# Kernel tuning notes

Hardware: AMD Instinct MI355X
Metric: run time of the kernel (lower is better)

Reference implementation:

```python
import jax, jax.numpy as jnp
from jax import lax
import numpy as np

NPOINT, RADIUS, NSAMPLE = 1024, 0.2, 32
MLP = [64, 64, 128]
IN_CH = 35  # 3 coord channels + 32 point features
EPS = 1e-5


def farthest_point_sample(xyz, npoint):
    # xyz: (B, N, 3) -> (B, npoint) int32. Deterministic start at index 0.
    B, N, _ = xyz.shape

    def step(carry, _):
        dist, farthest = carry  # (B,N), (B,)
        centroid = jnp.take_along_axis(xyz, farthest[:, None, None], axis=1)  # (B,1,3)
        d = jnp.sum((xyz - centroid) ** 2, axis=-1)  # (B,N)
        dist = jnp.minimum(dist, d)
        nxt = jnp.argmax(dist, axis=-1).astype(jnp.int32)
        return (dist, nxt), farthest

    init = (jnp.full((B, N), 1e10, xyz.dtype), jnp.zeros((B,), jnp.int32))
    _, idxs = lax.scan(step, init, None, length=npoint)
    return idxs.T  # (B, npoint)


def gather_points(points, idx):
    # points: (B, N, C); idx: (B, ...) int -> (B, ..., C)
    return jax.vmap(lambda p, i: p[i])(points, idx)


def query_ball_point(radius, nsample, xyz, new_xyz):
    # xyz: (B,N,3), new_xyz: (B,S,3) -> (B,S,nsample) int32
    B, N, _ = xyz.shape
    sqrdists = jnp.sum((new_xyz[:, :, None, :] - xyz[:, None, :, :]) ** 2, axis=-1)  # (B,S,N)
    group_idx = jnp.where(sqrdists > radius ** 2, N, jnp.arange(N, dtype=jnp.int32))
    group_idx = jnp.sort(group_idx, axis=-1)[:, :, :nsample]
    first = group_idx[:, :, :1]
    return jnp.where(group_idx == N, first, group_idx)


def sa_forward(xyz, points, params):
    B, N, C = xyz.shape
    fps_idx = farthest_point_sample(xyz, NPOINT)
    new_xyz = gather_points(xyz, fps_idx)  # (B,S,3)
    idx = query_ball_point(RADIUS, NSAMPLE, xyz, new_xyz)  # (B,S,K)
    grouped_xyz = gather_points(xyz, idx)  # (B,S,K,3)
    grouped_xyz_norm = grouped_xyz - new_xyz[:, :, None, :]
    grouped_points = gather_points(points, idx)  # (B,S,K,D)
    new_points = jnp.concatenate([grouped_xyz_norm, grouped_points], axis=-1)  # (B,S,K,Cin)
    x = new_points.transpose(0, 3, 2, 1)  # (B, Cin, K, S)
    for w, b, g, be in params:
        x = jnp.einsum('oi,biks->boks', w, x) + b[None, :, None, None]  # 1x1 conv
        mean = x.mean(axis=(0, 2, 3), keepdims=True)  # BatchNorm2d, training mode
        var = x.var(axis=(0, 2, 3), keepdims=True)
        x = (x - mean) / jnp.sqrt(var + EPS)
        x = jax.nn.relu(g[None, :, None, None] * x + be[None, :, None, None])
    new_points_out = x.max(axis=2)  # max over nsample -> (B, Cout, S)
    return new_xyz, new_points_out


def setup_inputs() -> dict:
    key = jax.random.key(0)
    ks = jax.random.split(key, 16)
    B, N, D = 16, 4096, 32
    inp = {
        'xyz': jax.random.uniform(ks[0], (B, N, 3), dtype=jnp.float32),
        'points': jax.random.normal(ks[1], (B, N, D), dtype=jnp.float32),
    }
    last = IN_CH
    for li, out_ch in enumerate(MLP):
        inp[f'w{li}'] = jax.random.normal(ks[2 + 4 * li], (out_ch, last), dtype=jnp.float32) * 0.05
        inp[f'b{li}'] = jnp.zeros((out_ch,), jnp.float32)
        inp[f'g{li}'] = jnp.ones((out_ch,), jnp.float32)
        inp[f'be{li}'] = jnp.zeros((out_ch,), jnp.float32)
        last = out_ch
    return inp


def reference(xyz, points, w0, b0, g0, be0, w1, b1, g1, be1, w2, b2, g2, be2):
    params = [(w0, b0, g0, be0), (w1, b1, g1, be1), (w2, b2, g2, be2)]
    return sa_forward(xyz, points, params)
```

## Files before the change

kernel.cpp:

```cpp
#include <hip/hip_runtime.h>
#include <hip/hip_bf16.h>
#include <stdint.h>

#pragma clang fp contract(off)

#define BATCH   16
#define NPTS    4096
#define NPOINT  1024
#define NSAMPLE 32
#define NPOS    (BATCH*NPOINT*NSAMPLE)
#define NBLK    (NPOS/128)
#define NGRP    (BATCH*NPOINT)
#define EPSV    1e-5f

typedef unsigned short ushort_t;
typedef unsigned int uint_t;
typedef unsigned long long u64;
typedef __attribute__((ext_vector_type(8))) short bf16x8;
typedef __attribute__((ext_vector_type(4))) float f32x4;
typedef __attribute__((ext_vector_type(2))) float f32x2;

__device__ inline ushort_t f2bf(float f) {
    uint_t u = __float_as_uint(f);
    u += 0x7fffu + ((u >> 16) & 1u);
    return (ushort_t)(u >> 16);
}
__device__ inline uint_t pkbf(float a, float b) {
    __hip_bfloat162 h = __float22bfloat162_rn(make_float2(a, b));
    uint_t r; __builtin_memcpy(&r, &h, 4); return r;
}
__device__ inline bf16x8 asbf(uint4 u) {
    bf16x8 v; __builtin_memcpy(&v, &u, 16); return v;
}
__device__ inline void unpack8(uint4 u, float* f) {
    f[0] = __uint_as_float(u.x << 16); f[1] = __uint_as_float(u.x & 0xffff0000u);
    f[2] = __uint_as_float(u.y << 16); f[3] = __uint_as_float(u.y & 0xffff0000u);
    f[4] = __uint_as_float(u.z << 16); f[5] = __uint_as_float(u.z & 0xffff0000u);
    f[6] = __uint_as_float(u.w << 16); f[7] = __uint_as_float(u.w & 0xffff0000u);
}

__global__ __launch_bounds__(256) void prep_w(const float* __restrict__ w0,
                                              const float* __restrict__ w1,
                                              const float* __restrict__ w2,
                                              ushort_t* __restrict__ Wp0,
                                              ushort_t* __restrict__ Wx0,
                                              ushort_t* __restrict__ Wp1,
                                              ushort_t* __restrict__ Wp2) {
    const int t = blockIdx.x * 256 + threadIdx.x;
    const int stride = gridDim.x * 256;
    for (int i = t; i < 64 * 32; i += stride) { int ch = i >> 5, k = i & 31; Wp0[i] = f2bf(w0[ch * 35 + 3 + k]); }
    for (int i = t; i < 64 * 4;  i += stride) { int ch = i >> 2, q = i & 3;  Wx0[i] = (q < 3) ? f2bf(w0[ch * 35 + q]) : (ushort_t)0; }
    for (int i = t; i < 64 * 64; i += stride) Wp1[i] = f2bf(w1[i]);
    for (int i = t; i < 128 * 64; i += stride) Wp2[i] = f2bf(w2[i]);
}

#define DPP_MAX_STAGE(CTRL) do {                                              \
    uint_t _lo2 = __builtin_amdgcn_update_dpp(lo, lo, CTRL, 0xf, 0xf, false); \
    uint_t _hi2 = __builtin_amdgcn_update_dpp(hi, hi, CTRL, 0xf, 0xf, false); \
    u64 _o = ((u64)_hi2 << 32) | _lo2;                                        \
    u64 _v = ((u64)hi << 32) | lo;                                            \
    bool _g = _o > _v;                                                        \
    lo = _g ? _lo2 : lo; hi = _g ? _hi2 : hi;                                 \
} while (0)

__global__ __launch_bounds__(256) void fps_kernel(const float* __restrict__ xyz,
                                                  float* __restrict__ new_xyz) {
    __shared__ float4 lxyz[NPTS];
    __shared__ u64 wbest[2][4];
    __shared__ int fpsidx[NPOINT];
    const int b = blockIdx.x;
    const int tid = threadIdx.x;
    const float* base = xyz + (size_t)b * NPTS * 3;
    for (int n = tid; n < NPTS; n += 256) {
        lxyz[n] = make_float4(base[3 * n], base[3 * n + 1], base[3 * n + 2], 0.f);
    }
    __syncthreads();

    f32x2 px[8], py[8], pz[8], dist[8];
    uint_t lowc[16];
#pragma unroll
    for (int j = 0; j < 8; j++) {
// ... 51 lines not shown
        u64 b2 = wbest[par][2], b3 = wbest[par][3];
        u64 m01 = b0 > b1 ? b0 : b1;
        u64 m23 = b2 > b3 ? b2 : b3;
        u64 bb = m01 > m23 ? m01 : m23;
        cur = (int)(~(uint_t)bb) & (NPTS - 1);
        if (tid == 0) fpsidx[it] = cur;
    }
    __syncthreads();
    float* ob = new_xyz + (size_t)b * NPOINT * 3;
    for (int s = tid; s < NPOINT; s += 256) {
        float4 v = lxyz[fpsidx[s]];
        ob[3 * s + 0] = v.x; ob[3 * s + 1] = v.y; ob[3 * s + 2] = v.z;
    }
}

__global__ __launch_bounds__(256) void ballq_kernel(const float* __restrict__ xyz,
                                                    const float* __restrict__ new_xyz,
                                                    int* __restrict__ gidx) {
    const int gw = (int)((blockIdx.x * 256 + threadIdx.x) >> 6);
    const int lane = threadIdx.x & 63;
    const int b = gw / NPOINT, s = gw % NPOINT;
    const float* nb = new_xyz + ((size_t)b * NPOINT + s) * 3;
    const float cx = nb[0], cy = nb[1], cz = nb[2];
    const float* xb = xyz + (size_t)b * NPTS * 3;
    const float r2 = (float)(0.2 * 0.2);
    int cnt = 0;
    int first = -1;
    int* out = gidx + (size_t)gw * NSAMPLE;
    for (int j0 = 0; j0 < NPTS; j0 += 64) {
        int j = j0 + lane;
        float dx = __fsub_rn(xb[j * 3 + 0], cx);
        float dy = __fsub_rn(xb[j * 3 + 1], cy);
        float dz = __fsub_rn(xb[j * 3 + 2], cz);
        float d = __fadd_rn(__fadd_rn(__fmul_rn(dx, dx), __fmul_rn(dy, dy)),
                            __fmul_rn(dz, dz));
        bool pred = !(d > r2);
        u64 mask = __ballot(pred);
        if (first < 0 && mask != 0ull) first = j0 + (__ffsll((long long)mask) - 1);
        int before = __popcll(mask & ((1ull << lane) - 1ull));
        int slot = cnt + before;
        if (pred && slot < NSAMPLE) out[slot] = j;
        cnt += (int)__popcll(mask);
        if (cnt >= NSAMPLE) break;
    }
    if (cnt < NSAMPLE) {
        if (lane >= cnt && lane < NSAMPLE) out[lane] = first;
    }
}

__global__ __launch_bounds__(256) void conv1_mfma(const float* __restrict__ xyz,
                                                  const float* __restrict__ points,
                                                  const float* __restrict__ new_xyz,
                                                  const int* __restrict__ gidx,
                                                  const ushort_t* __restrict__ Wp0,
                                                  const ushort_t* __restrict__ Wx0,
                                                  const float* __restrict__ bias,
                                                  ushort_t* __restrict__ Y,
                                                  float* __restrict__ part_s,
                                                  float* __restrict__ part_q) {
    const int lane = threadIdx.x & 63, wid = threadIdx.x >> 6;
    const int l15 = lane & 15, quad = lane >> 4;
    const int p0 = blockIdx.x * 128 + wid * 32;

    bf16x8 Bp[4], Bx[4];
#pragma unroll
    for (int nt = 0; nt < 4; nt++) {
        const int ch = nt * 16 + l15;
        Bp[nt] = *(const bf16x8*)(Wp0 + (size_t)ch * 32 + quad * 8);
        uint4 bx = {0u, 0u, 0u, 0u};
        if (quad == 0) {
            uint2 wv = *(const uint2*)(Wx0 + ch * 4);
            bx.x = wv.x; bx.y = wv.y;
        }
        Bx[nt] = asbf(bx);
    }
    f32x4 acc[2][4];
#pragma unroll
    for (int mt = 0; mt < 2; mt++)
#pragma unroll
        for (int nt = 0; nt < 4; nt++) acc[mt][nt] = (f32x4){0.f, 0.f, 0.f, 0.f};

#pragma unroll
    for (int mt = 0; mt < 2; mt++) {
        const int p = p0 + mt * 16 + l15;
        const int b = p >> 15, s = (p & 32767) >> 5;
        const int j = gidx[p];
        const float* pr = points + ((size_t)(b * NPTS + j)) * 32 + quad * 8;
        float4 pa = *(const float4*)pr;
        float4 pb4 = *(const float4*)(pr + 4);
        uint4 ap;
        ap.x = pkbf(pa.x, pa.y);  ap.y = pkbf(pa.z, pa.w);
        ap.z = pkbf(pb4.x, pb4.y); ap.w = pkbf(pb4.z, pb4.w);
        bf16x8 Ap = asbf(ap);
        uint4 ax = {0u, 0u, 0u, 0u};
        if (quad == 0) {
            const float* xp = xyz + ((size_t)(b * NPTS + j)) * 3;
            const float* nz = new_xyz + ((size_t)(b * NPOINT + s)) * 3;
            float d0 = xp[0] - nz[0], d1 = xp[1] - nz[1], d2 = xp[2] - nz[2];
            ax.x = pkbf(d0, d1);
            ax.y = pkbf(d2, 0.f);
        }
        bf16x8 Ax = asbf(ax);
#pragma unroll
        for (int nt = 0; nt < 4; nt++) {
            acc[mt][nt] = __builtin_amdgcn_mfma_f32_16x16x32_bf16(Ap, Bp[nt], acc[mt][nt], 0, 0, 0);
            acc[mt][nt] = __builtin_amdgcn_mfma_f32_16x16x32_bf16(Ax, Bx[nt], acc[mt][nt], 0, 0, 0);
        }
    }
    float s_[4], q_[4];
#pragma unroll
    for (int nt = 0; nt < 4; nt++) { s_[nt] = 0.f; q_[nt] = 0.f; }
#pragma unroll
    for (int nt = 0; nt < 4; nt++) {
        const int ch = nt * 16 + l15;
        const float bs = bias[ch];
#pragma unroll
        for (int mt = 0; mt < 2; mt++) {
            const int pb = p0 + mt * 16 + quad * 4;
            float x0 = acc[mt][nt][0] + bs, x1 = acc[mt][nt][1] + bs;
            float x2 = acc[mt][nt][2] + bs, x3 = acc[mt][nt][3] + bs;
            uint_t p01 = pkbf(x0, x1), p23 = pkbf(x2, x3);
            Y[(size_t)(pb + 0) * 64 + ch] = (ushort_t)(p01 & 0xffffu);
            Y[(size_t)(pb + 1) * 64 + ch] = (ushort_t)(p01 >> 16);
            Y[(size_t)(pb + 2) * 64 + ch] = (ushort_t)(p23 & 0xffffu);
            Y[(size_t)(pb + 3) * 64 + ch] = (ushort_t)(p23 >> 16);
            float v0 = __uint_as_float(p01 << 16), v1 = __uint_as_float(p01 & 0xffff0000u);
            float v2 = __uint_as_float(p23 << 16), v3 = __uint_as_float(p23 & 0xffff0000u);
            s_[nt] += (v0 + v1) + (v2 + v3);
            q_[nt] += (v0 * v0 + v1 * v1) + (v2 * v2 + v3 * v3);
        }
    }
#pragma unroll
    for (int nt = 0; nt < 4; nt++) {
        s_[nt] += __shfl_xor(s_[nt], 16, 64); s_[nt] += __shfl_xor(s_[nt], 32, 64);
        q_[nt] += __shfl_xor(q_[nt], 16, 64); q_[nt] += __shfl_xor(q_[nt], 32, 64);
    }
    __shared__ float reds[4][4][16], redq[4][4][16];
    if (lane < 16) {
#pragma unroll
        for (int nt = 0; nt < 4; nt++) { reds[wid][nt][lane] = s_[nt]; redq[wid][nt][lane] = q_[nt]; }
    }
    __syncthreads();
    if (threadIdx.x < 16) {
#pragma unroll
        for (int nt = 0; nt < 4; nt++) {
            float ss = 0.f, qq = 0.f;
#pragma unroll
            for (int w = 0; w < 4; w++) { ss += reds[w][nt][threadIdx.x]; qq += redq[w][nt][threadIdx.x]; }
            const int ch = nt * 16 + threadIdx.x;
            part_s[(size_t)ch * NBLK + blockIdx.x] = ss;
            part_q[(size_t)ch * NBLK + blockIdx.x] = qq;
        }
    }
}

__global__ __launch_bounds__(256) void conv2_mfma(const ushort_t* __restrict__ Yin,
                                                  const float* __restrict__ scale,
                                                  const float* __restrict__ shift,
                                                  const ushort_t* __restrict__ Wp,
                                                  const float* __restrict__ bias,
                                                  ushort_t* __restrict__ Yout,
                                                  float* __restrict__ part_s,
                                                  float* __restrict__ part_q) {
    constexpr int IN = 64, OUT = 64, NT = 4;
    const int lane = threadIdx.x & 63, wid = threadIdx.x >> 6;
    const int l15 = lane & 15, quad = lane >> 4;
    const int p0 = blockIdx.x * 128 + wid * 32;

    float sc[2][8], sh[2][8];
#pragma unroll
    for (int kq = 0; kq < 2; kq++) {
        const int i0 = kq * 32 + quad * 8;
#pragma unroll
        for (int q = 0; q < 8; q++) { sc[kq][q] = scale[i0 + q]; sh[kq][q] = shift[i0 + q]; }
    }
    bf16x8 Bf[NT][2];
#pragma unroll
    for (int nt = 0; nt < NT; nt++)
#pragma unroll
        for (int kq = 0; kq < 2; kq++)
            Bf[nt][kq] = *(const bf16x8*)(Wp + (size_t)(nt * 16 + l15) * IN + kq * 32 + quad * 8);

    bf16x8 Af[2][2];
#pragma unroll
    for (int mt = 0; mt < 2; mt++)
#pragma unroll
        for (int kq = 0; kq < 2; kq++) {
            const ushort_t* yr = Yin + (size_t)(p0 + mt * 16 + l15) * IN + kq * 32 + quad * 8;
            uint4 u = *(const uint4*)yr;
            float f[8]; unpack8(u, f);
            float g0 = fmaxf(fmaf(f[0], sc[kq][0], sh[kq][0]), 0.f);
            float g1 = fmaxf(fmaf(f[1], sc[kq][1], sh[kq][1]), 0.f);
            float g2 = fmaxf(fmaf(f[2], sc[kq][2], sh[kq][2]), 0.f);
            float g3 = fmaxf(fmaf(f[3], sc[kq][3], sh[kq][3]), 0.f);
            float g4 = fmaxf(fmaf(f[4], sc[kq][4], sh[kq][4]), 0.f);
            float g5 = fmaxf(fmaf(f[5], sc[kq][5], sh[kq][5]), 0.f);
            float g6 = fmaxf(fmaf(f[6], sc[kq][6], sh[kq][6]), 0.f);
            float g7 = fmaxf(fmaf(f[7], sc[kq][7], sh[kq][7]), 0.f);
            uint4 a;
            a.x = pkbf(g0, g1); a.y = pkbf(g2, g3);
            a.z = pkbf(g4, g5); a.w = pkbf(g6, g7);
            Af[mt][kq] = asbf(a);
        }

    f32x4 acc[2][NT];
#pragma unroll
    for (int mt = 0; mt < 2; mt++)
#pragma unroll
        for (int nt = 0; nt < NT; nt++) acc[mt][nt] = (f32x4){0.f, 0.f, 0.f, 0.f};
#pragma unroll
    for (int mt = 0; mt < 2; mt++)
#pragma unroll
        for (int nt = 0; nt < NT; nt++) {
            acc[mt][nt] = __builtin_amdgcn_mfma_f32_16x16x32_bf16(Af[mt][0], Bf[nt][0], acc[mt][nt], 0, 0, 0);
            acc[mt][nt] = __builtin_amdgcn_mfma_f32_16x16x32_bf16(Af[mt][1], Bf[nt][1], acc[mt][nt], 0, 0, 0);
        }
    float s_[NT], q_[NT];
#pragma unroll
    for (int nt = 0; nt < NT; nt++) { s_[nt] = 0.f; q_[nt] = 0.f; }
#pragma unroll
    for (int nt = 0; nt < NT; nt++) {
        const int ch = nt * 16 + l15;
        const float bs = bias[ch];
#pragma unroll
        for (int mt = 0; mt < 2; mt++) {
            const int pb = p0 + mt * 16 + quad * 4;
            float x0 = acc[mt][nt][0] + bs, x1 = acc[mt][nt][1] + bs;
            float x2 = acc[mt][nt][2] + bs, x3 = acc[mt][nt][3] + bs;
            uint_t p01 = pkbf(x0, x1), p23 = pkbf(x2, x3);
            Yout[(size_t)(pb + 0) * OUT + ch] = (ushort_t)(p01 & 0xffffu);
            Yout[(size_t)(pb + 1) * OUT + ch] = (ushort_t)(p01 >> 16);
            Yout[(size_t)(pb + 2) * OUT + ch] = (ushort_t)(p23 & 0xffffu);
            Yout[(size_t)(pb + 3) * OUT + ch] = (ushort_t)(p23 >> 16);
            float v0 = __uint_as_float(p01 << 16), v1 = __uint_as_float(p01 & 0xffff0000u);
            float v2 = __uint_as_float(p23 << 16), v3 = __uint_as_float(p23 & 0xffff0000u);
            s_[nt] += (v0 + v1) + (v2 + v3);
            q_[nt] += (v0 * v0 + v1 * v1) + (v2 * v2 + v3 * v3);
        }
    }
#pragma unroll
    for (int nt = 0; nt < NT; nt++) {
        s_[nt] += __shfl_xor(s_[nt], 16, 64); s_[nt] += __shfl_xor(s_[nt], 32, 64);
        q_[nt] += __shfl_xor(q_[nt], 16, 64); q_[nt] += __shfl_xor(q_[nt], 32, 64);
    }
    __shared__ float reds[4][NT][16], redq[4][NT][16];
    if (lane < 16) {
#pragma unroll
        for (int nt = 0; nt < NT; nt++) { reds[wid][nt][lane] = s_[nt]; redq[wid][nt][lane] = q_[nt]; }
    }
    __syncthreads();
    if (threadIdx.x < 16) {
#pragma unroll
        for (int nt = 0; nt < NT; nt++) {
            float ss = 0.f, qq = 0.f;
#pragma unroll
            for (int w = 0; w < 4; w++) { ss += reds[w][nt][threadIdx.x]; qq += redq[w][nt][threadIdx.x]; }
            const int ch = nt * 16 + threadIdx.x;
            part_s[(size_t)ch * NBLK + blockIdx.x] = ss;
            part_q[(size_t)ch * NBLK + blockIdx.x] = qq;
        }
    }
}

__global__ __launch_bounds__(256) void conv3_mfma(const ushort_t* __restrict__ Yin,
                                                  const float* __restrict__ scale,
                                                  const float* __restrict__ shift,
                                                  const ushort_t* __restrict__ Wp,
                                                  const float* __restrict__ bias,
                                                  float* __restrict__ xmax,
                                                  float* __restrict__ xmin,
                                                  float* __restrict__ part_s,
                                                  float* __restrict__ part_q) {
    constexpr int IN = 64, NT = 8;
    const int lane = threadIdx.x & 63, wid = threadIdx.x >> 6;
    const int l15 = lane & 15, quad = lane >> 4;
    const int p0 = blockIdx.x * 128 + wid * 32;
    const int g = p0 >> 5;

    float sc[2][8], sh[2][8];
#pragma unroll
    for (int kq = 0; kq < 2; kq++) {
        const int i0 = kq * 32 + quad * 8;
#pragma unroll
        for (int q = 0; q < 8; q++) { sc[kq][q] = scale[i0 + q]; sh[kq][q] = shift[i0 + q]; }
    }
    bf16x8 Bf[NT][2];
#pragma unroll
    for (int nt = 0; nt < NT; nt++)
#pragma unroll
        for (int kq = 0; kq < 2; kq++)
            Bf[nt][kq] = *(const bf16x8*)(Wp + (size_t)(nt * 16 + l15) * IN + kq * 32 + quad * 8);

    bf16x8 Af[2][2];
#pragma unroll
    for (int mt = 0; mt < 2; mt++)
#pragma unroll
        for (int kq = 0; kq < 2; kq++) {
            const ushort_t* yr = Yin + (size_t)(p0 + mt * 16 + l15) * IN + kq * 32 + quad * 8;
            uint4 u = *(const uint4*)yr;
            float f[8]; unpack8(u, f);
            float g0 = fmaxf(fmaf(f[0], sc[kq][0], sh[kq][0]), 0.f);
            float g1 = fmaxf(fmaf(f[1], sc[kq][1], sh[kq][1]), 0.f);
            float g2 = fmaxf(fmaf(f[2], sc[kq][2], sh[kq][2]), 0.f);
            float g3 = fmaxf(fmaf(f[3], sc[kq][3], sh[kq][3]), 0.f);
            float g4 = fmaxf(fmaf(f[4], sc[kq][4], sh[kq][4]), 0.f);
            float g5 = fmaxf(fmaf(f[5], sc[kq][5], sh[kq][5]), 0.f);
            float g6 = fmaxf(fmaf(f[6], sc[kq][6], sh[kq][6]), 0.f);
            float g7 = fmaxf(fmaf(f[7], sc[kq][7], sh[kq][7]), 0.f);
            uint4 a;
            a.x = pkbf(g0, g1); a.y = pkbf(g2, g3);
            a.z = pkbf(g4, g5); a.w = pkbf(g6, g7);
            Af[mt][kq] = asbf(a);
        }

    f32x4 acc[2][NT];
#pragma unroll
    for (int mt = 0; mt < 2; mt++)
#pragma unroll
        for (int nt = 0; nt < NT; nt++) acc[mt][nt] = (f32x4){0.f, 0.f, 0.f, 0.f};
#pragma unroll
    for (int mt = 0; mt < 2; mt++)
#pragma unroll
        for (int nt = 0; nt < NT; nt++) {
            acc[mt][nt] = __builtin_amdgcn_mfma_f32_16x16x32_bf16(Af[mt][0], Bf[nt][0], acc[mt][nt], 0, 0, 0);
            acc[mt][nt] = __builtin_amdgcn_mfma_f32_16x16x32_bf16(Af[mt][1], Bf[nt][1], acc[mt][nt], 0, 0, 0);
        }
    float s_[NT], q_[NT], xm[NT], xn[NT];
#pragma unroll
    for (int nt = 0; nt < NT; nt++) { s_[nt] = 0.f; q_[nt] = 0.f; xm[nt] = -3e38f; xn[nt] = 3e38f; }
#pragma unroll
    for (int nt = 0; nt < NT; nt++) {
        const float bs = bias[nt * 16 + l15];
#pragma unroll
        for (int mt = 0; mt < 2; mt++) {
#pragma unroll
            for (int r = 0; r < 4; r++) {
                float x = acc[mt][nt][r] + bs;
                s_[nt] += x; q_[nt] += x * x;
                xm[nt] = fmaxf(xm[nt], x); xn[nt] = fminf(xn[nt], x);
            }
        }
    }
#pragma unroll
    for (int nt = 0; nt < NT; nt++) {
        s_[nt] += __shfl_xor(s_[nt], 16, 64); s_[nt] += __shfl_xor(s_[nt], 32, 64);
        q_[nt] += __shfl_xor(q_[nt], 16, 64); q_[nt] += __shfl_xor(q_[nt], 32, 64);
        xm[nt] = fmaxf(xm[nt], __shfl_xor(xm[nt], 16, 64));
        xm[nt] = fmaxf(xm[nt], __shfl_xor(xm[nt], 32, 64));
        xn[nt] = fminf(xn[nt], __shfl_xor(xn[nt], 16, 64));
        xn[nt] = fminf(xn[nt], __shfl_xor(xn[nt], 32, 64));
    }
    if (quad == 0) {
#pragma unroll
        for (int nt = 0; nt < NT; nt++) {
            const int ch = nt * 16 + l15;
            xmax[(size_t)g * 128 + ch] = xm[nt];
            xmin[(size_t)g * 128 + ch] = xn[nt];
        }
    }
    __shared__ float reds[4][NT][16], redq[4][NT][16];
    if (lane < 16) {
#pragma unroll
        for (int nt = 0; nt < NT; nt++) { reds[wid][nt][lane] = s_[nt]; redq[wid][nt][lane] = q_[nt]; }
    }
    __syncthreads();
    if (threadIdx.x < 16) {
#pragma unroll
        for (int nt = 0; nt < NT; nt++) {
            float ss = 0.f, qq = 0.f;
#pragma unroll
            for (int w = 0; w < 4; w++) { ss += reds[w][nt][threadIdx.x]; qq += redq[w][nt][threadIdx.x]; }
            const int ch = nt * 16 + threadIdx.x;
            part_s[(size_t)ch * NBLK + blockIdx.x] = ss;
            part_q[(size_t)ch * NBLK + blockIdx.x] = qq;
        }
    }
}

__global__ __launch_bounds__(256) void reduce_finalize(const float* __restrict__ part_s,
                                                       const float* __restrict__ part_q,
                                                       const float* __restrict__ g,
                                                       const float* __restrict__ be,
                                                       float* __restrict__ scale,
                                                       float* __restrict__ shift) {
    const int ch = blockIdx.x;
    const float* p1 = part_s + (size_t)ch * NBLK;
    const float* p2 = part_q + (size_t)ch * NBLK;
    float s = 0.f, q = 0.f;
    for (int i = threadIdx.x; i < NBLK; i += 256) { s += p1[i]; q += p2[i]; }
#pragma unroll
    for (int m = 1; m < 64; m <<= 1) { s += __shfl_xor(s, m, 64); q += __shfl_xor(q, m, 64); }
    __shared__ float ls[4], lq[4];
    const int lane = threadIdx.x & 63, wid = threadIdx.x >> 6;
    if (lane == 0) { ls[wid] = s; lq[wid] = q; }
    __syncthreads();
    if (threadIdx.x == 0) {
        float ssum = ls[0] + ls[1] + ls[2] + ls[3];
        float qsum = lq[0] + lq[1] + lq[2] + lq[3];
        float mean = ssum * (1.f / (float)NPOS);
        float var = qsum * (1.f / (float)NPOS) - mean * mean;
        float inv = 1.f / sqrtf(var + EPSV);
        float sc = g[ch] * inv;
        scale[ch] = sc;
        shift[ch] = be[ch] - mean * sc;
// ... 37 lines not shown
    const float* w1 = (const float*)d_in[6];
    const float* b1 = (const float*)d_in[7];
    const float* g1 = (const float*)d_in[8];
    const float* be1 = (const float*)d_in[9];
    const float* w2 = (const float*)d_in[10];
    const float* b2 = (const float*)d_in[11];
    const float* g2 = (const float*)d_in[12];
    const float* be2 = (const float*)d_in[13];

    float* out = (float*)d_out;
    float* new_xyz = out;
    float* final_out = out + BATCH * NPOINT * 3;

    char* ws = (char*)d_ws;
    const size_t MB = 1024u * 1024u;
    const size_t o_gidx = 0;
    const size_t o_y2 = 2 * MB;
    const size_t o_y1 = o_y2 + (size_t)NPOS * 64 * 2;
    const size_t o_params = o_y1 + (size_t)NPOS * 64 * 2;
    const size_t o_parts = o_params + 4096;
    const size_t o_w = o_parts + 4 * MB;
    const size_t o_xm = o_w + 64 * 1024;
    const size_t o_xn = o_xm + (size_t)NGRP * 128 * 4;

    int* gidx = (int*)(ws + o_gidx);
    ushort_t* Y1 = (ushort_t*)(ws + o_y1);
    ushort_t* Y2 = (ushort_t*)(ws + o_y2);
    float* pr = (float*)(ws + o_params);
    float* scale1 = pr + 0, *shift1 = pr + 64;
    float* scale2 = pr + 128, *shift2 = pr + 192;
    float* scale3 = pr + 256, *shift3 = pr + 384;
    float* part_s = (float*)(ws + o_parts);
    float* part_q = part_s + (size_t)128 * NBLK;
    ushort_t* Wp0 = (ushort_t*)(ws + o_w);
    ushort_t* Wx0 = Wp0 + 64 * 32;
    ushort_t* Wp1 = Wx0 + 64 * 4;
    ushort_t* Wp2 = Wp1 + 64 * 64;
    float* xmax = (float*)(ws + o_xm);
    float* xmin = (float*)(ws + o_xn);

    prep_w<<<8, 256, 0, stream>>>(w0, w1, w2, Wp0, Wx0, Wp1, Wp2);
    fps_kernel<<<BATCH, 256, 0, stream>>>(xyz, new_xyz);
    ballq_kernel<<<(BATCH * NPOINT) / 4, 256, 0, stream>>>(xyz, new_xyz, gidx);
    conv1_mfma<<<NBLK, 256, 0, stream>>>(xyz, points, new_xyz, gidx, Wp0, Wx0, b0, Y1, part_s, part_q);
    reduce_finalize<<<64, 256, 0, stream>>>(part_s, part_q, g0, be0, scale1, shift1);
    conv2_mfma<<<NBLK, 256, 0, stream>>>(Y1, scale1, shift1, Wp1, b1, Y2, part_s, part_q);
    reduce_finalize<<<64, 256, 0, stream>>>(part_s, part_q, g1, be1, scale2, shift2);
    conv3_mfma<<<NBLK, 256, 0, stream>>>(Y2, scale2, shift2, Wp2, b2, xmax, xmin, part_s, part_q);
    reduce_finalize<<<128, 256, 0, stream>>>(part_s, part_q, g2, be2, scale3, shift3);
    final2_kernel<<<128, 256, 0, stream>>>(xmax, xmin, scale3, shift3, final_out);
}
```

Before: 890.9 us.

## Fuse ball query into conv1, fold weight prep into FPS, persistent conv blocks

Moves the ball-query search into conv1 so neighbour indices live in shared memory and never round-trip through global memory. Weight bf16 conversion now runs in an extra block of the FPS launch, and a separate ball-query kernel is dropped. All three conv kernels now launch 512 blocks that each loop over 8 tiles, which shrinks the partial-sum arrays and simplifies the reduction. The cost is lower parallelism: 512 blocks with serial ball-query scans inside conv1 may leave the GPU underused.

Measured after the change: 928.9 us. 4.3% more time.

```diff
diff --git a/kernel.cpp b/kernel.cpp
--- a/kernel.cpp
+++ b/kernel.cpp
@@ -9,7 +9,7 @@
 #define NPOINT  1024
 #define NSAMPLE 32
 #define NPOS    (BATCH*NPOINT*NSAMPLE)
-#define NBLK    (NPOS/128)
+#define NBLKC   512
 #define NGRP    (BATCH*NPOINT)
 #define EPSV    1e-5f
 
@@ -37,21 +37,6 @@
     f[2] = __uint_as_float(u.y << 16); f[3] = __uint_as_float(u.y & 0xffff0000u);
     f[4] = __uint_as_float(u.z << 16); f[5] = __uint_as_float(u.z & 0xffff0000u);
     f[6] = __uint_as_float(u.w << 16); f[7] = __uint_as_float(u.w & 0xffff0000u);
-}
-
-__global__ __launch_bounds__(256) void prep_w(const float* __restrict__ w0,
-                                              const float* __restrict__ w1,
-                                              const float* __restrict__ w2,
-                                              ushort_t* __restrict__ Wp0,
-                                              ushort_t* __restrict__ Wx0,
-                                              ushort_t* __restrict__ Wp1,
-                                              ushort_t* __restrict__ Wp2) {
-    const int t = blockIdx.x * 256 + threadIdx.x;
-    const int stride = gridDim.x * 256;
-    for (int i = t; i < 64 * 32; i += stride) { int ch = i >> 5, k = i & 31; Wp0[i] = f2bf(w0[ch * 35 + 3 + k]); }
-    for (int i = t; i < 64 * 4;  i += stride) { int ch = i >> 2, q = i & 3;  Wx0[i] = (q < 3) ? f2bf(w0[ch * 35 + q]) : (ushort_t)0; }
-    for (int i = t; i < 64 * 64; i += stride) Wp1[i] = f2bf(w1[i]);
-    for (int i = t; i < 128 * 64; i += stride) Wp2[i] = f2bf(w2[i]);
 }
 
 #define DPP_MAX_STAGE(CTRL) do {                                              \
@@ -64,7 +49,22 @@
 } while (0)
 
 __global__ __launch_bounds__(256) void fps_kernel(const float* __restrict__ xyz,
-                                                  float* __restrict__ new_xyz) {
+                                                  float* __restrict__ new_xyz,
+                                                  const float* __restrict__ w0,
+                                                  const float* __restrict__ w1,
+                                                  const float* __restrict__ w2,
+                                                  ushort_t* __restrict__ Wp0,
+                                                  ushort_t* __restrict__ Wx0,
+                                                  ushort_t* __restrict__ Wp1,
+                                                  ushort_t* __restrict__ Wp2) {
+    if (blockIdx.x == 16) {
+        const int t = threadIdx.x;
+        for (int i = t; i < 64 * 32; i += 256) { int ch = i >> 5, k = i & 31; Wp0[i] = f2bf(w0[ch * 35 + 3 + k]); }
+        for (int i = t; i < 64 * 4;  i += 256) { int ch = i >> 2, q = i & 3;  Wx0[i] = (q < 3) ? f2bf(w0[ch * 35 + q]) : (ushort_t)0; }
+        for (int i = t; i < 64 * 64; i += 256) Wp1[i] = f2bf(w1[i]);
+        for (int i = t; i < 128 * 64; i += 256) Wp2[i] = f2bf(w2[i]);
+        return;
+    }
     __shared__ float4 lxyz[NPTS];
     __shared__ u64 wbest[2][4];
     __shared__ int fpsidx[NPOINT];
@@ -146,53 +146,19 @@
     }
 }
 
-__global__ __launch_bounds__(256) void ballq_kernel(const float* __restrict__ xyz,
-                                                    const float* __restrict__ new_xyz,
-                                                    int* __restrict__ gidx) {
-    const int gw = (int)((blockIdx.x * 256 + threadIdx.x) >> 6);
-    const int lane = threadIdx.x & 63;
-    const int b = gw / NPOINT, s = gw % NPOINT;
-    const float* nb = new_xyz + ((size_t)b * NPOINT + s) * 3;
-    const float cx = nb[0], cy = nb[1], cz = nb[2];
-    const float* xb = xyz + (size_t)b * NPTS * 3;
-    const float r2 = (float)(0.2 * 0.2);
-    int cnt = 0;
-    int first = -1;
-    int* out = gidx + (size_t)gw * NSAMPLE;
-    for (int j0 = 0; j0 < NPTS; j0 += 64) {
-        int j = j0 + lane;
-        float dx = __fsub_rn(xb[j * 3 + 0], cx);
-        float dy = __fsub_rn(xb[j * 3 + 1], cy);
-        float dz = __fsub_rn(xb[j * 3 + 2], cz);
-        float d = __fadd_rn(__fadd_rn(__fmul_rn(dx, dx), __fmul_rn(dy, dy)),
-                            __fmul_rn(dz, dz));
-        bool pred = !(d > r2);
-        u64 mask = __ballot(pred);
-        if (first < 0 && mask != 0ull) first = j0 + (__ffsll((long long)mask) - 1);
-        int before = __popcll(mask & ((1ull << lane) - 1ull));
-        int slot = cnt + before;
-        if (pred && slot < NSAMPLE) out[slot] = j;
-        cnt += (int)__popcll(mask);
-        if (cnt >= NSAMPLE) break;
-    }
-    if (cnt < NSAMPLE) {
-        if (lane >= cnt && lane < NSAMPLE) out[lane] = first;
-    }
-}
-
 __global__ __launch_bounds__(256) void conv1_mfma(const float* __restrict__ xyz,
                                                   const float* __restrict__ points,
                                                   const float* __restrict__ new_xyz,
-                                                  const int* __restrict__ gidx,
                                                   const ushort_t* __restrict__ Wp0,
                                                   const ushort_t* __restrict__ Wx0,
                                                   const float* __restrict__ bias,
                                                   ushort_t* __restrict__ Y,
                                                   float* __restrict__ part_s,
                                                   float* __restrict__ part_q) {
+    __shared__ int wbuf[4][NSAMPLE];
+    __shared__ float reds[4][4][16], redq[4][4][16];
     const int lane = threadIdx.x & 63, wid = threadIdx.x >> 6;
     const int l15 = lane & 15, quad = lane >> 4;
-    const int p0 = blockIdx.x * 128 + wid * 32;
 
     bf16x8 Bp[4], Bx[4];
 #pragma unroll
@@ -206,60 +172,88 @@
         }
         Bx[nt] = asbf(bx);
     }
-    f32x4 acc[2][4];
-#pragma unroll
-    for (int mt = 0; mt < 2; mt++)
-#pragma unroll
-        for (int nt = 0; nt < 4; nt++) acc[mt][nt] = (f32x4){0.f, 0.f, 0.f, 0.f};
-
-#pragma unroll
-    for (int mt = 0; mt < 2; mt++) {
-        const int p = p0 + mt * 16 + l15;
-        const int b = p >> 15, s = (p & 32767) >> 5;
-        const int j = gidx[p];
-        const float* pr = points + ((size_t)(b * NPTS + j)) * 32 + quad * 8;
-        float4 pa = *(const float4*)pr;
-        float4 pb4 = *(const float4*)(pr + 4);
-        uint4 ap;
-        ap.x = pkbf(pa.x, pa.y);  ap.y = pkbf(pa.z, pa.w);
-        ap.z = pkbf(pb4.x, pb4.y); ap.w = pkbf(pb4.z, pb4.w);
-        bf16x8 Ap = asbf(ap);
-        uint4 ax = {0u, 0u, 0u, 0u};
-        if (quad == 0) {
-            const float* xp = xyz + ((size_t)(b * NPTS + j)) * 3;
-            const float* nz = new_xyz + ((size_t)(b * NPOINT + s)) * 3;
-            float d0 = xp[0] - nz[0], d1 = xp[1] - nz[1], d2 = xp[2] - nz[2];
-            ax.x = pkbf(d0, d1);
-            ax.y = pkbf(d2, 0.f);
-        }
-        bf16x8 Ax = asbf(ax);
+    float bs[4];
+#pragma unroll
+    for (int nt = 0; nt < 4; nt++) bs[nt] = bias[nt * 16 + l15];
+    float s_[4], q_[4];
+#pragma unroll
+    for (int nt = 0; nt < 4; nt++) { s_[nt] = 0.f; q_[nt] = 0.f; }
+    const float r2 = (float)(0.2 * 0.2);
+
+    for (int it = 0; it < 8; it++) {
+        const int p0 = (blockIdx.x + NBLKC * it) * 128 + wid * 32;
+        const int g = p0 >> 5;
+        const int b = g >> 10, s = g & 1023;
+        const float* nb = new_xyz + ((size_t)(b * NPOINT + s)) * 3;
+        const float cx = nb[0], cy = nb[1], cz = nb[2];
+        const float* xb = xyz + (size_t)b * NPTS * 3;
+        int cnt = 0, first = -1;
+        for (int j0 = 0; j0 < NPTS; j0 += 64) {
+            int j = j0 + lane;
+            float dx = __fsub_rn(xb[j * 3 + 0], cx);
+            float dy = __fsub_rn(xb[j * 3 + 1], cy);
+            float dz = __fsub_rn(xb[j * 3 + 2], cz);
+            float d = __fadd_rn(__fadd_rn(__fmul_rn(dx, dx), __fmul_rn(dy, dy)),
+                                __fmul_rn(dz, dz));
+            bool pred = !(d > r2);
+            u64 mask = __ballot(pred);
+            if (first < 0 && mask != 0ull) first = j0 + (__ffsll((long long)mask) - 1);
+            int before = __popcll(mask & ((1ull << lane) - 1ull));
+            int slot = cnt + before;
+            if (pred && slot < NSAMPLE) wbuf[wid][slot] = j;
+            cnt += (int)__popcll(mask);
+            if (cnt >= NSAMPLE) break;
+        }
+        if (cnt < NSAMPLE) {
+            if (lane >= cnt && lane < NSAMPLE) wbuf[wid][lane] = first;
+        }
+        f32x4 acc[2][4];
+#pragma unroll
+        for (int mt = 0; mt < 2; mt++)
+#pragma unroll
+            for (int nt = 0; nt < 4; nt++) acc[mt][nt] = (f32x4){0.f, 0.f, 0.f, 0.f};
+#pragma unroll
+        for (int mt = 0; mt < 2; mt++) {
+            const int j = wbuf[wid][mt * 16 + l15];
+            const float* pr = points + ((size_t)(b * NPTS + j)) * 32 + quad * 8;
+            float4 pa = *(const float4*)pr;
+            float4 pb4 = *(const float4*)(pr + 4);
+            uint4 ap;
+            ap.x = pkbf(pa.x, pa.y);  ap.y = pkbf(pa.z, pa.w);
+            ap.z = pkbf(pb4.x, pb4.y); ap.w = pkbf(pb4.z, pb4.w);
+            bf16x8 Ap = asbf(ap);
+            uint4 ax = {0u, 0u, 0u, 0u};
+            if (quad == 0) {
+                const float* xp = xyz + ((size_t)(b * NPTS + j)) * 3;
+                float d0 = xp[0] - cx, d1 = xp[1] - cy, d2 = xp[2] - cz;
+                ax.x = pkbf(d0, d1);
+                ax.y = pkbf(d2, 0.f);
+            }
+            bf16x8 Ax = asbf(ax);
+#pragma unroll
+            for (int nt = 0; nt < 4; nt++) {
+                acc[mt][nt] = __builtin_amdgcn_mfma_f32_16x16x32_bf16(Ap, Bp[nt], acc[mt][nt], 0, 0, 0);
+                acc[mt][nt] = __builtin_amdgcn_mfma_f32_16x16x32_bf16(Ax, Bx[nt], acc[mt][nt], 0, 0, 0);
+            }
+        }
 #pragma unroll
         for (int nt = 0; nt < 4; nt++) {
-            acc[mt][nt] = __builtin_amdgcn_mfma_f32_16x16x32_bf16(Ap, Bp[nt], acc[mt][nt], 0, 0, 0);
-            acc[mt][nt] = __builtin_amdgcn_mfma_f32_16x16x32_bf16(Ax, Bx[nt], acc[mt][nt], 0, 0, 0);
-        }
-    }
-    float s_[4], q_[4];
-#pragma unroll
-    for (int nt = 0; nt < 4; nt++) { s_[nt] = 0.f; q_[nt] = 0.f; }
-#pragma unroll
-    for (int nt = 0; nt < 4; nt++) {
-        const int ch = nt * 16 + l15;
-        const float bs = bias[ch];
-#pragma unroll
-        for (int mt = 0; mt < 2; mt++) {
-            const int pb = p0 + mt * 16 + quad * 4;
-            float x0 = acc[mt][nt][0] + bs, x1 = acc[mt][nt][1] + bs;
-            float x2 = acc[mt][nt][2] + bs, x3 = acc[mt][nt][3] + bs;
-            uint_t p01 = pkbf(x0, x1), p23 = pkbf(x2, x3);
-            Y[(size_t)(pb + 0) * 64 + ch] = (ushort_t)(p01 & 0xffffu);
-            Y[(size_t)(pb + 1) * 64 + ch] = (ushort_t)(p01 >> 16);
-            Y[(size_t)(pb + 2) * 64 + ch] = (ushort_t)(p23 & 0xffffu);
-            Y[(size_t)(pb + 3) * 64 + ch] = (ushort_t)(p23 >> 16);
-            float v0 = __uint_as_float(p01 << 16), v1 = __uint_as_float(p01 & 0xffff0000u);
-            float v2 = __uint_as_float(p23 << 16), v3 = __uint_as_float(p23 & 0xffff0000u);
-            s_[nt] += (v0 + v1) + (v2 + v3);
-            q_[nt] += (v0 * v0 + v1 * v1) + (v2 * v2 + v3 * v3);
+            const int ch = nt * 16 + l15;
+#pragma unroll
+            for (int mt = 0; mt < 2; mt++) {
+                const int pb = p0 + mt * 16 + quad * 4;
+                float x0 = acc[mt][nt][0] + bs[nt], x1 = acc[mt][nt][1] + bs[nt];
+                float x2 = acc[mt][nt][2] + bs[nt], x3 = acc[mt][nt][3] + bs[nt];
+                uint_t p01 = pkbf(x0, x1), p23 = pkbf(x2, x3);
+                Y[(size_t)(pb + 0) * 64 + ch] = (ushort_t)(p01 & 0xffffu);
+                Y[(size_t)(pb + 1) * 64 + ch] = (ushort_t)(p01 >> 16);
+                Y[(size_t)(pb + 2) * 64 + ch] = (ushort_t)(p23 & 0xffffu);
+                Y[(size_t)(pb + 3) * 64 + ch] = (ushort_t)(p23 >> 16);
+                float v0 = __uint_as_float(p01 << 16), v1 = __uint_as_float(p01 & 0xffff0000u);
+                float v2 = __uint_as_float(p23 << 16), v3 = __uint_as_float(p23 & 0xffff0000u);
+                s_[nt] += (v0 + v1) + (v2 + v3);
+                q_[nt] += (v0 * v0 + v1 * v1) + (v2 * v2 + v3 * v3);
+            }
         }
     }
 #pragma unroll
@@ -267,7 +261,6 @@
         s_[nt] += __shfl_xor(s_[nt], 16, 64); s_[nt] += __shfl_xor(s_[nt], 32, 64);
         q_[nt] += __shfl_xor(q_[nt], 16, 64); q_[nt] += __shfl_xor(q_[nt], 32, 64);
     }
-    __shared__ float reds[4][4][16], redq[4][4][16];
     if (lane < 16) {
 #pragma unroll
         for (int nt = 0; nt < 4; nt++) { reds[wid][nt][lane] = s_[nt]; redq[wid][nt][lane] = q_[nt]; }
@@ -280,8 +273,8 @@
 #pragma unroll
             for (int w = 0; w < 4; w++) { ss += reds[w][nt][threadIdx.x]; qq += redq[w][nt][threadIdx.x]; }
             const int ch = nt * 16 + threadIdx.x;
-            part_s[(size_t)ch * NBLK + blockIdx.x] = ss;
-            part_q[(size_t)ch * NBLK + blockIdx.x] = qq;
+            part_s[(size_t)ch * NBLKC + blockIdx.x] = ss;
+            part_q[(size_t)ch * NBLKC + blockIdx.x] = qq;
         }
     }
 }
@@ -295,9 +288,9 @@
                                                   float* __restrict__ part_s,
                                                   float* __restrict__ part_q) {
     constexpr int IN = 64, OUT = 64, NT = 4;
+    __shared__ float reds[4][NT][16], redq[4][NT][16];
     const int lane = threadIdx.x & 63, wid = threadIdx.x >> 6;
     const int l15 = lane & 15, quad = lane >> 4;
-    const int p0 = blockIdx.x * 128 + wid * 32;
 
     float sc[2][8], sh[2][8];
 #pragma unroll
@@ -312,62 +305,66 @@
 #pragma unroll
         for (int kq = 0; kq < 2; kq++)
             Bf[nt][kq] = *(const bf16x8*)(Wp + (size_t)(nt * 16 + l15) * IN + kq * 32 + quad * 8);
-
-    bf16x8 Af[2][2];
-#pragma unroll
-    for (int mt = 0; mt < 2; mt++)
-#pragma unroll
-        for (int kq = 0; kq < 2; kq++) {
-            const ushort_t* yr = Yin + (size_t)(p0 + mt * 16 + l15) * IN + kq * 32 + quad * 8;
-            uint4 u = *(const uint4*)yr;
-            float f[8]; unpack8(u, f);
-            float g0 = fmaxf(fmaf(f[0], sc[kq][0], sh[kq][0]), 0.f);
-            float g1 = fmaxf(fmaf(f[1], sc[kq][1], sh[kq][1]), 0.f);
-            float g2 = fmaxf(fmaf(f[2], sc[kq][2], sh[kq][2]), 0.f);
-            float g3 = fmaxf(fmaf(f[3], sc[kq][3], sh[kq][3]), 0.f);
-            float g4 = fmaxf(fmaf(f[4], sc[kq][4], sh[kq][4]), 0.f);
-            float g5 = fmaxf(fmaf(f[5], sc[kq][5], sh[kq][5]), 0.f);
-            float g6 = fmaxf(fmaf(f[6], sc[kq][6], sh[kq][6]), 0.f);
-            float g7 = fmaxf(fmaf(f[7], sc[kq][7], sh[kq][7]), 0.f);
-            uint4 a;
-            a.x = pkbf(g0, g1); a.y = pkbf(g2, g3);
-            a.z = pkbf(g4, g5); a.w = pkbf(g6, g7);
-            Af[mt][kq] = asbf(a);
-        }
-
-    f32x4 acc[2][NT];
-#pragma unroll
-    for (int mt = 0; mt < 2; mt++)
-#pragma unroll
-        for (int nt = 0; nt < NT; nt++) acc[mt][nt] = (f32x4){0.f, 0.f, 0.f, 0.f};
-#pragma unroll
-    for (int mt = 0; mt < 2; mt++)
+    float bs[NT];
+#pragma unroll
+    for (int nt = 0; nt < NT; nt++) bs[nt] = bias[nt * 16 + l15];
+    float s_[NT], q_[NT];
+#pragma unroll
+    for (int nt = 0; nt < NT; nt++) { s_[nt] = 0.f; q_[nt] = 0.f; }
+
+    for (int it = 0; it < 8; it++) {
+        const int p0 = (blockIdx.x + NBLKC * it) * 128 + wid * 32;
+        bf16x8 Af[2][2];
+#pragma unroll
+        for (int mt = 0; mt < 2; mt++)
+#pragma unroll
+            for (int kq = 0; kq < 2; kq++) {
+                const ushort_t* yr = Yin + (size_t)(p0 + mt * 16 + l15) * IN + kq * 32 + quad * 8;
+                uint4 u = *(const uint4*)yr;
+                float f[8]; unpack8(u, f);
+                float g0 = fmaxf(fmaf(f[0], sc[kq][0], sh[kq][0]), 0.f);
+                float g1 = fmaxf(fmaf(f[1], sc[kq][1], sh[kq][1]), 0.f);
+                float g2 = fmaxf(fmaf(f[2], sc[kq][2], sh[kq][2]), 0.f);
+                float g3 = fmaxf(fmaf(f[3], sc[kq][3], sh[kq][3]), 0.f);
+                float g4 = fmaxf(fmaf(f[4], sc[kq][4], sh[kq][4]), 0.f);
+                float g5 = fmaxf(fmaf(f[5], sc[kq][5], sh[kq][5]), 0.f);
+                float g6 = fmaxf(fmaf(f[6], sc[kq][6], sh[kq][6]), 0.f);
+                float g7 = fmaxf(fmaf(f[7], sc[kq][7], sh[kq][7]), 0.f);
+                uint4 a;
+                a.x = pkbf(g0, g1); a.y = pkbf(g2, g3);
+                a.z = pkbf(g4, g5); a.w = pkbf(g6, g7);
+                Af[mt][kq] = asbf(a);
+            }
+        f32x4 acc[2][NT];
+#pragma unroll
+        for (int mt = 0; mt < 2; mt++)
+#pragma unroll
+            for (int nt = 0; nt < NT; nt++) acc[mt][nt] = (f32x4){0.f, 0.f, 0.f, 0.f};
+#pragma unroll
+        for (int mt = 0; mt < 2; mt++)
+#pragma unroll
+            for (int nt = 0; nt < NT; nt++) {
+                acc[mt][nt] = __builtin_amdgcn_mfma_f32_16x16x32_bf16(Af[mt][0], Bf[nt][0], acc[mt][nt], 0, 0, 0);
+                acc[mt][nt] = __builtin_amdgcn_mfma_f32_16x16x32_bf16(Af[mt][1], Bf[nt][1], acc[mt][nt], 0, 0, 0);
+            }
 #pragma unroll
         for (int nt = 0; nt < NT; nt++) {
-            acc[mt][nt] = __builtin_amdgcn_mfma_f32_16x16x32_bf16(Af[mt][0], Bf[nt][0], acc[mt][nt], 0, 0, 0);
-            acc[mt][nt] = __builtin_amdgcn_mfma_f32_16x16x32_bf16(Af[mt][1], Bf[nt][1], acc[mt][nt], 0, 0, 0);
-        }
-    float s_[NT], q_[NT];
-#pragma unroll
-    for (int nt = 0; nt < NT; nt++) { s_[nt] = 0.f; q_[nt] = 0.f; }
-#pragma unroll
-    for (int nt = 0; nt < NT; nt++) {
-        const int ch = nt * 16 + l15;
-        const float bs = bias[ch];
-#pragma unroll
-        for (int mt = 0; mt < 2; mt++) {
-            const int pb = p0 + mt * 16 + quad * 4;
-            float x0 = acc[mt][nt][0] + bs, x1 = acc[mt][nt][1] + bs;
-            float x2 = acc[mt][nt][2] + bs, x3 = acc[mt][nt][3] + bs;
-            uint_t p01 = pkbf(x0, x1), p23 = pkbf(x2, x3);
-            Yout[(size_t)(pb + 0) * OUT + ch] = (ushort_t)(p01 & 0xffffu);
-            Yout[(size_t)(pb + 1) * OUT + ch] = (ushort_t)(p01 >> 16);
-            Yout[(size_t)(pb + 2) * OUT + ch] = (ushort_t)(p23 & 0xffffu);
-            Yout[(size_t)(pb + 3) * OUT + ch] = (ushort_t)(p23 >> 16);
-            float v0 = __uint_as_float(p01 << 16), v1 = __uint_as_float(p01 & 0xffff0000u);
-            float v2 = __uint_as_float(p23 << 16), v3 = __uint_as_float(p23 & 0xffff0000u);
-            s_[nt] += (v0 + v1) + (v2 + v3);
-            q_[nt] += (v0 * v0 + v1 * v1) + (v2 * v2 + v3 * v3);
+            const int ch = nt * 16 + l15;
+#pragma unroll
+            for (int mt = 0; mt < 2; mt++) {
+                const int pb = p0 + mt * 16 + quad * 4;
+                float x0 = acc[mt][nt][0] + bs[nt], x1 = acc[mt][nt][1] + bs[nt];
+                float x2 = acc[mt][nt][2] + bs[nt], x3 = acc[mt][nt][3] + bs[nt];
+                uint_t p01 = pkbf(x0, x1), p23 = pkbf(x2, x3);
+                Yout[(size_t)(pb + 0) * OUT + ch] = (ushort_t)(p01 & 0xffffu);
+                Yout[(size_t)(pb + 1) * OUT + ch] = (ushort_t)(p01 >> 16);
+                Yout[(size_t)(pb + 2) * OUT + ch] = (ushort_t)(p23 & 0xffffu);
+                Yout[(size_t)(pb + 3) * OUT + ch] = (ushort_t)(p23 >> 16);
+                float v0 = __uint_as_float(p01 << 16), v1 = __uint_as_float(p01 & 0xffff0000u);
+                float v2 = __uint_as_float(p23 << 16), v3 = __uint_as_float(p23 & 0xffff0000u);
+                s_[nt] += (v0 + v1) + (v2 + v3);
+                q_[nt] += (v0 * v0 + v1 * v1) + (v2 * v2 + v3 * v3);
+            }
         }
     }
 #pragma unroll
@@ -375,7 +372,6 @@
         s_[nt] += __shfl_xor(s_[nt], 16, 64); s_[nt] += __shfl_xor(s_[nt], 32, 64);
         q_[nt] += __shfl_xor(q_[nt], 16, 64); q_[nt] += __shfl_xor(q_[nt], 32, 64);
     }
-    __shared__ float reds[4][NT][16], redq[4][NT][16];
     if (lane < 16) {
 #pragma unroll
         for (int nt = 0; nt < NT; nt++) { reds[wid][nt][lane] = s_[nt]; redq[wid][nt][lane] = q_[nt]; }
@@ -388,8 +384,8 @@
 #pragma unroll
             for (int w = 0; w < 4; w++) { ss += reds[w][nt][threadIdx.x]; qq += redq[w][nt][threadIdx.x]; }
             const int ch = nt * 16 + threadIdx.x;
-            part_s[(size_t)ch * NBLK + blockIdx.x] = ss;
-            part_q[(size_t)ch * NBLK + blockIdx.x] = qq;
+            part_s[(size_t)ch * NBLKC + blockIdx.x] = ss;
+            part_q[(size_t)ch * NBLKC + blockIdx.x] = qq;
         }
     }
 }
@@ -404,10 +400,9 @@
                                                   float* __restrict__ part_s,
                                                   float* __restrict__ part_q) {
     constexpr int IN = 64, NT = 8;
+    __shared__ float reds[4][NT][16], redq[4][NT][16];
     const int lane = threadIdx.x & 63, wid = threadIdx.x >> 6;
     const int l15 = lane & 15, quad = lane >> 4;
-    const int p0 = blockIdx.x * 128 + wid * 32;
-    const int g = p0 >> 5;
 
     float sc[2][8], sh[2][8];
 #pragma unroll
@@ -422,54 +417,77 @@
 #pragma unroll
         for (int kq = 0; kq < 2; kq++)
             Bf[nt][kq] = *(const bf16x8*)(Wp + (size_t)(nt * 16 + l15) * IN + kq * 32 + quad * 8);
-
-    bf16x8 Af[2][2];
-#pragma unroll
-    for (int mt = 0; mt < 2; mt++)
-#pragma unroll
-        for (int kq = 0; kq < 2; kq++) {
-            const ushort_t* yr = Yin + (size_t)(p0 + mt * 16 + l15) * IN + kq * 32 + quad * 8;
-            uint4 u = *(const uint4*)yr;
-            float f[8]; unpack8(u, f);
-            float g0 = fmaxf(fmaf(f[0], sc[kq][0], sh[kq][0]), 0.f);
-            float g1 = fmaxf(fmaf(f[1], sc[kq][1], sh[kq][1]), 0.f);
-            float g2 = fmaxf(fmaf(f[2], sc[kq][2], sh[kq][2]), 0.f);
-            float g3 = fmaxf(fmaf(f[3], sc[kq][3], sh[kq][3]), 0.f);
-            float g4 = fmaxf(fmaf(f[4], sc[kq][4], sh[kq][4]), 0.f);
-            float g5 = fmaxf(fmaf(f[5], sc[kq][5], sh[kq][5]), 0.f);
-            float g6 = fmaxf(fmaf(f[6], sc[kq][6], sh[kq][6]), 0.f);
-            float g7 = fmaxf(fmaf(f[7], sc[kq][7], sh[kq][7]), 0.f);
-            uint4 a;
-            a.x = pkbf(g0, g1); a.y = pkbf(g2, g3);
-            a.z = pkbf(g4, g5); a.w = pkbf(g6, g7);
-            Af[mt][kq] = asbf(a);
-        }
-
-    f32x4 acc[2][NT];
-#pragma unroll
-    for (int mt = 0; mt < 2; mt++)
-#pragma unroll
-        for (int nt = 0; nt < NT; nt++) acc[mt][nt] = (f32x4){0.f, 0.f, 0.f, 0.f};
-#pragma unroll
-    for (int mt = 0; mt < 2; mt++)
+    float bs[NT];
+#pragma unroll
+    for (int nt = 0; nt < NT; nt++) bs[nt] = bias[nt * 16 + l15];
+    float s_[NT], q_[NT];
+#pragma unroll
+    for (int nt = 0; nt < NT; nt++) { s_[nt] = 0.f; q_[nt] = 0.f; }
+
+    for (int it = 0; it < 8; it++) {
+        const int p0 = (blockIdx.x + NBLKC * it) * 128 + wid * 32;
+        const int g = p0 >> 5;
+        bf16x8 Af[2][2];
+#pragma unroll
+        for (int mt = 0; mt < 2; mt++)
+#pragma unroll
+            for (int kq = 0; kq < 2; kq++) {
+                const ushort_t* yr = Yin + (size_t)(p0 + mt * 16 + l15) * IN + kq * 32 + quad * 8;
+                uint4 u = *(const uint4*)yr;
+                float f[8]; unpack8(u, f);
+                float g0 = fmaxf(fmaf(f[0], sc[kq][0], sh[kq][0]), 0.f);
+                float g1 = fmaxf(fmaf(f[1], sc[kq][1], sh[kq][1]), 0.f);
+                float g2 = fmaxf(fmaf(f[2], sc[kq][2], sh[kq][2]), 0.f);
+                float g3 = fmaxf(fmaf(f[3], sc[kq][3], sh[kq][3]), 0.f);
+                float g4 = fmaxf(fmaf(f[4], sc[kq][4], sh[kq][4]), 0.f);
+                float g5 = fmaxf(fmaf(f[5], sc[kq][5], sh[kq][5]), 0.f);
+                float g6 = fmaxf(fmaf(f[6], sc[kq][6], sh[kq][6]), 0.f);
+                float g7 = fmaxf(fmaf(f[7], sc[kq][7], sh[kq][7]), 0.f);
+                uint4 a;
+                a.x = pkbf(g0, g1); a.y = pkbf(g2, g3);
+                a.z = pkbf(g4, g5); a.w = pkbf(g6, g7);
+                Af[mt][kq] = asbf(a);
+            }
+        f32x4 acc[2][NT];
+#pragma unroll
+        for (int mt = 0; mt < 2; mt++)
+#pragma unroll
+            for (int nt = 0; nt < NT; nt++) acc[mt][nt] = (f32x4){0.f, 0.f, 0.f, 0.f};
+#pragma unroll
+        for (int mt = 0; mt < 2; mt++)
+#pragma unroll
+            for (int nt = 0; nt < NT; nt++) {
+                acc[mt][nt] = __builtin_amdgcn_mfma_f32_16x16x32_bf16(Af[mt][0], Bf[nt][0], acc[mt][nt], 0, 0, 0);
+                acc[mt][nt] = __builtin_amdgcn_mfma_f32_16x16x32_bf16(Af[mt][1], Bf[nt][1], acc[mt][nt], 0, 0, 0);
+            }
+        float xm[NT], xn[NT];
+#pragma unroll
+        for (int nt = 0; nt < NT; nt++) { xm[nt] = -3e38f; xn[nt] = 3e38f; }
 #pragma unroll
         for (int nt = 0; nt < NT; nt++) {
-            acc[mt][nt] = __builtin_amdgcn_mfma_f32_16x16x32_bf16(Af[mt][0], Bf[nt][0], acc[mt][nt], 0, 0, 0);
-            acc[mt][nt] = __builtin_amdgcn_mfma_f32_16x16x32_bf16(Af[mt][1], Bf[nt][1], acc[mt][nt], 0, 0, 0);
-        }
-    float s_[NT], q_[NT], xm[NT], xn[NT];
-#pragma unroll
-    for (int nt = 0; nt < NT; nt++) { s_[nt] = 0.f; q_[nt] = 0.f; xm[nt] = -3e38f; xn[nt] = 3e38f; }
-#pragma unroll
-    for (int nt = 0; nt < NT; nt++) {
-        const float bs = bias[nt * 16 + l15];
-#pragma unroll
-        for (int mt = 0; mt < 2; mt++) {
-#pragma unroll
-            for (int r = 0; r < 4; r++) {
-                float x = acc[mt][nt][r] + bs;
-                s_[nt] += x; q_[nt] += x * x;
-                xm[nt] = fmaxf(xm[nt], x); xn[nt] = fminf(xn[nt], x);
+#pragma unroll
+            for (int mt = 0; mt < 2; mt++) {
+#pragma unroll
+                for (int r = 0; r < 4; r++) {
+                    float x = acc[mt][nt][r] + bs[nt];
+                    s_[nt] += x; q_[nt] += x * x;
+                    xm[nt] = fmaxf(xm[nt], x); xn[nt] = fminf(xn[nt], x);
+                }
+            }
+        }
+#pragma unroll
+        for (int nt = 0; nt < NT; nt++) {
+            xm[nt] = fmaxf(xm[nt], __shfl_xor(xm[nt], 16, 64));
+            xm[nt] = fmaxf(xm[nt], __shfl_xor(xm[nt], 32, 64));
+            xn[nt] = fminf(xn[nt], __shfl_xor(xn[nt], 16, 64));
+            xn[nt] = fminf(xn[nt], __shfl_xor(xn[nt], 32, 64));
+        }
+        if (quad == 0) {
+#pragma unroll
+            for (int nt = 0; nt < NT; nt++) {
+                const int ch = nt * 16 + l15;
+                xmax[(size_t)g * 128 + ch] = xm[nt];
+                xmin[(size_t)g * 128 + ch] = xn[nt];
             }
         }
     }
@@ -477,20 +495,7 @@
     for (int nt = 0; nt < NT; nt++) {
         s_[nt] += __shfl_xor(s_[nt], 16, 64); s_[nt] += __shfl_xor(s_[nt], 32, 64);
         q_[nt] += __shfl_xor(q_[nt], 16, 64); q_[nt] += __shfl_xor(q_[nt], 32, 64);
-        xm[nt] = fmaxf(xm[nt], __shfl_xor(xm[nt], 16, 64));
-        xm[nt] = fmaxf(xm[nt], __shfl_xor(xm[nt], 32, 64));
-        xn[nt] = fminf(xn[nt], __shfl_xor(xn[nt], 16, 64));
-        xn[nt] = fminf(xn[nt], __shfl_xor(xn[nt], 32, 64));
-    }
-    if (quad == 0) {
-#pragma unroll
-        for (int nt = 0; nt < NT; nt++) {
-            const int ch = nt * 16 + l15;
-            xmax[(size_t)g * 128 + ch] = xm[nt];
-            xmin[(size_t)g * 128 + ch] = xn[nt];
-        }
-    }
-    __shared__ float reds[4][NT][16], redq[4][NT][16];
+    }
     if (lane < 16) {
 #pragma unroll
         for (int nt = 0; nt < NT; nt++) { reds[wid][nt][lane] = s_[nt]; redq[wid][nt][lane] = q_[nt]; }
@@ -503,8 +508,8 @@
 #pragma unroll
             for (int w = 0; w < 4; w++) { ss += reds[w][nt][threadIdx.x]; qq += redq[w][nt][threadIdx.x]; }
             const int ch = nt * 16 + threadIdx.x;
-            part_s[(size_t)ch * NBLK + blockIdx.x] = ss;
-            part_q[(size_t)ch * NBLK + blockIdx.x] = qq;
+            part_s[(size_t)ch * NBLKC + blockIdx.x] = ss;
+            part_q[(size_t)ch * NBLKC + blockIdx.x] = qq;
         }
     }
 }
@@ -516,10 +521,10 @@
                                                        float* __restrict__ scale,
                                                        float* __restrict__ shift) {
     const int ch = blockIdx.x;
-    const float* p1 = part_s + (size_t)ch * NBLK;
-    const float* p2 = part_q + (size_t)ch * NBLK;
-    float s = 0.f, q = 0.f;
-    for (int i = threadIdx.x; i < NBLK; i += 256) { s += p1[i]; q += p2[i]; }
+    const float* p1 = part_s + (size_t)ch * NBLKC;
+    const float* p2 = part_q + (size_t)ch * NBLKC;
+    float s = p1[threadIdx.x] + p1[threadIdx.x + 256];
+    float q = p2[threadIdx.x] + p2[threadIdx.x + 256];
 #pragma unroll
     for (int m = 1; m < 64; m <<= 1) { s += __shfl_xor(s, m, 64); q += __shfl_xor(q, m, 64); }
     __shared__ float ls[4], lq[4];
@@ -587,16 +592,14 @@
 
     char* ws = (char*)d_ws;
     const size_t MB = 1024u * 1024u;
-    const size_t o_gidx = 0;
-    const size_t o_y2 = 2 * MB;
+    const size_t o_y2 = 0;
     const size_t o_y1 = o_y2 + (size_t)NPOS * 64 * 2;
     const size_t o_params = o_y1 + (size_t)NPOS * 64 * 2;
     const size_t o_parts = o_params + 4096;
-    const size_t o_w = o_parts + 4 * MB;
+    const size_t o_w = o_parts + 1 * MB;
     const size_t o_xm = o_w + 64 * 1024;
     const size_t o_xn = o_xm + (size_t)NGRP * 128 * 4;
 
-    int* gidx = (int*)(ws + o_gidx);
     ushort_t* Y1 = (ushort_t*)(ws + o_y1);
     ushort_t* Y2 = (ushort_t*)(ws + o_y2);
     float* pr = (float*)(ws + o_params);
@@ -604,7 +607,7 @@
     float* scale2 = pr + 128, *shift2 = pr + 192;
     float* scale3 = pr + 256, *shift3 = pr + 384;
     float* part_s = (float*)(ws + o_parts);
-    float* part_q = part_s + (size_t)128 * NBLK;
+    float* part_q = part_s + (size_t)128 * NBLKC;
     ushort_t* Wp0 = (ushort_t*)(ws + o_w);
     ushort_t* Wx0 = Wp0 + 64 * 32;
     ushort_t* Wp1 = Wx0 + 64 * 4;
@@ -612,14 +615,12 @@
     float* xmax = (float*)(ws + o_xm);
     float* xmin = (float*)(ws + o_xn);
 
-    prep_w<<<8, 256, 0, stream>>>(w0, w1, w2, Wp0, Wx0, Wp1, Wp2);
-    fps_kernel<<<BATCH, 256, 0, stream>>>(xyz, new_xyz);
-    ballq_kernel<<<(BATCH * NPOINT) / 4, 256, 0, stream>>>(xyz, new_xyz, gidx);
-    conv1_mfma<<<NBLK, 256, 0, stream>>>(xyz, points, new_xyz, gidx, Wp0, Wx0, b0, Y1, part_s, part_q);
+    fps_kernel<<<17, 256, 0, stream>>>(xyz, new_xyz, w0, w1, w2, Wp0, Wx0, Wp1, Wp2);
+    conv1_mfma<<<NBLKC, 256, 0, stream>>>(xyz, points, new_xyz, Wp0, Wx0, b0, Y1, part_s, part_q);
     reduce_finalize<<<64, 256, 0, stream>>>(part_s, part_q, g0, be0, scale1, shift1);
-    conv2_mfma<<<NBLK, 256, 0, stream>>>(Y1, scale1, shift1, Wp1, b1, Y2, part_s, part_q);
+    conv2_mfma<<<NBLKC, 256, 0, stream>>>(Y1, scale1, shift1, Wp1, b1, Y2, part_s, part_q);
     reduce_finalize<<<64, 256, 0, stream>>>(part_s, part_q, g1, be1, scale2, shift2);
-    conv3_mfma<<<NBLK, 256, 0, stream>>>(Y2, scale2, shift2, Wp2, b2, xmax, xmin, part_s, part_q);
+    conv3_mfma<<<NBLKC, 256, 0, stream>>>(Y2, scale2, shift2, Wp2, b2, xmax, xmin, part_s, part_q);
     reduce_finalize<<<128, 256, 0, stream>>>(part_s, part_q, g2, be2, scale3, shift3);
     final2_kernel<<<128, 256, 0, stream>>>(xmax, xmin, scale3, shift3, final_out);
 }
```
